# Kernel optimization log

Hardware: AMD Instinct MI355X
Metric: run time of the kernel (lower is better)

## Reference

```python
import jax, jax.numpy as jnp
import numpy as np

B, N, E = 64, 4096, 32768
F_IN, H = 12, 64
K1 = int(np.ceil(0.8 * N))    # TopKPooling ratio=0.8 -> 3277
K2 = int(np.ceil(0.8 * K1))   # -> 2622


def _lin(key, o, i):
    s = 1.0 / np.sqrt(i)
    return jax.random.uniform(key, (o, i), jnp.float32, -s, s)


def setup_inputs() -> dict:
    key = jax.random.key(0)
    ks = jax.random.split(key, 16)
    return {
        "x": jax.random.normal(ks[0], (B, N, F_IN), jnp.float32),
        "edge_index": jax.random.randint(ks[1], (B, 2, E), 0, N),
        # GraphConv 1: lin_rel (with bias) on aggregated msgs, lin_root (no bias)
        "W1_rel": _lin(ks[2], H, F_IN),
        "b1": jnp.zeros((H,), jnp.float32),
        "W1_root": _lin(ks[3], H, F_IN),
        # TopKPooling 1 projection vector
        "p1": jax.random.normal(ks[4], (H,), jnp.float32),
        # GraphConv 2
        "W2_rel": _lin(ks[5], H, H),
        "b2": jnp.zeros((H,), jnp.float32),
        "W2_root": _lin(ks[6], H, H),
        "p2": jax.random.normal(ks[7], (H,), jnp.float32),
        # heads
        "Wa1": _lin(ks[8], 64, 128),
        "ba1": jnp.zeros((64,), jnp.float32),
        "Wa5": _lin(ks[9], 10, 64),
        "ba5": jnp.zeros((10,), jnp.float32),
    }


def _graph_conv(x, src, dst, emask, Wr, br, Wn, n):
    # PyG GraphConv: lin_rel(sum_{j->i} x_j) + lin_root(x_i); masked edges send 0
    msg = x[src] * emask[:, None]                      # [E, d]
    agg = jax.ops.segment_sum(msg, dst, num_segments=n)  # [n, d]
    return agg @ Wr.T + br + x @ Wn.T


def _topk_pool(x, src, dst, emask, p, k):
    # score = x.p/||p||; keep top-k nodes, gate by tanh(score); mask dropped edges
    n = x.shape[0]
    score = (x @ p) / jnp.linalg.norm(p)
    vals, perm = jax.lax.top_k(score, k)
    xk = x[perm] * jnp.tanh(vals)[:, None]
    pos = jnp.full((n,), -1, jnp.int32).at[perm].set(jnp.arange(k, dtype=jnp.int32))
    ns, nd = pos[src], pos[dst]
    valid = (ns >= 0) & (nd >= 0) & (emask > 0)
    return xk, jnp.where(valid, ns, 0), jnp.where(valid, nd, 0), valid.astype(x.dtype)


def reference(x, edge_index, W1_rel, b1, W1_root, p1, W2_rel, b2, W2_root, p2, Wa1, ba1, Wa5, ba5):
    def per_graph(xg, eig):
        src, dst = eig[0], eig[1]
        emask = jnp.ones((src.shape[0],), xg.dtype)
        h = jax.nn.relu(_graph_conv(xg, src, dst, emask, W1_rel, b1, W1_root, N))
        h, src, dst, emask = _topk_pool(h, src, dst, emask, p1, K1)
        x1 = jnp.concatenate([h.max(axis=0), h.mean(axis=0)])   # gmp || gap -> [128]
        h = jax.nn.relu(_graph_conv(h, src, dst, emask, W2_rel, b2, W2_root, K1))
        h, src, dst, emask = _topk_pool(h, src, dst, emask, p2, K2)
        x2 = jnp.concatenate([h.max(axis=0), h.mean(axis=0)])
        return x1 + x2

    feats = jax.vmap(per_graph)(x, edge_index)                  # [B, 128]
    a1 = jax.nn.relu(feats @ Wa1.T + ba1)
    a5 = a1 @ Wa5.T + ba5                                       # [B, 10]
    # F.softmax(dim=0).unsqueeze(0): softmax ACROSS graphs, then add leading dim
    return jax.nn.softmax(a5, axis=0)[None]                     # [1, B, 10]
```

## Files before the change

kernel.cpp:

```cpp
#include <hip/hip_runtime.h>
#include <float.h>
#include <math.h>

#define BB 64
#define NN 4096
#define EE 32768
#define FIN 12
#define HD 64
#define KK1 3277
#define KK2 2622
#define TB1 52
#define RB2 16

__global__ __launch_bounds__(1024) void k_csr(const int* __restrict__ ei,
    int* __restrict__ row_ofs, int* __restrict__ esrc, int g0) {
  __shared__ int cnt[NN];
  __shared__ int part[1024];
  int s = blockIdx.x, g = g0 + s, t = threadIdx.x;
  const int* src = ei + (size_t)g * 2 * EE;
  const int* dst = src + EE;
  for (int i = t; i < NN; i += 1024) cnt[i] = 0;
  __syncthreads();
  for (int e = t; e < EE; e += 1024) atomicAdd(&cnt[dst[e]], 1);
  __syncthreads();
  int c0 = cnt[t * 4], c1 = cnt[t * 4 + 1], c2 = cnt[t * 4 + 2], c3 = cnt[t * 4 + 3];
  int tot = c0 + c1 + c2 + c3;
  part[t] = tot;
  __syncthreads();
  for (int off = 1; off < 1024; off <<= 1) {
    int v = part[t];
    int add = (t >= off) ? part[t - off] : 0;
    __syncthreads();
    part[t] = v + add;
    __syncthreads();
  }
  int base = part[t] - tot;
  int b0 = base, b1 = base + c0, b2 = b1 + c1, b3 = b2 + c2;
  cnt[t * 4] = b0; cnt[t * 4 + 1] = b1; cnt[t * 4 + 2] = b2; cnt[t * 4 + 3] = b3;
  int* RO = row_ofs + (size_t)s * (NN + 1);
  RO[t * 4] = b0; RO[t * 4 + 1] = b1; RO[t * 4 + 2] = b2; RO[t * 4 + 3] = b3;
  if (t == 0) RO[NN] = EE;
  __syncthreads();
  int* ES = esrc + (size_t)s * EE;
  for (int e = t; e < EE; e += 1024) {
    int p = atomicAdd(&cnt[dst[e]], 1);
    ES[p] = src[e];
  }
}

__global__ __launch_bounds__(256, 4) void k_h1f(const float* __restrict__ x,
    const int* __restrict__ row_ofs, const int* __restrict__ esrc,
    const float* __restrict__ W1r, const float* __restrict__ b1,
    const float* __restrict__ W1n, const float* __restrict__ p1,
    float* __restrict__ h1, float* __restrict__ score1, int g0, int G8) {
  __shared__ float sCol[32][257];
  int tid = threadIdx.x;
  int b = blockIdx.x, s, nb;
  if (G8 > 0) { int hi = b >> 3; s = (b & 7) * G8 + hi / 16; nb = hi % 16; }
  else { s = b >> 4; nb = b & 15; }
  int node = nb * 256 + tid;
  int g = g0 + s;
  float nq = 0.f;
#pragma unroll 8
  for (int k = 0; k < 64; k++) nq += p1[k] * p1[k];
  float inv_norm = 1.0f / sqrtf(nq);
  const int* RO = row_ofs + (size_t)s * (NN + 1);
  const int* ES = esrc + (size_t)s * EE;
  const float4* X4 = (const float4*)(x + (size_t)g * NN * FIN);
  int r0 = RO[node], r1 = RO[node + 1];
  float a[FIN];
#pragma unroll
  for (int f = 0; f < FIN; f++) a[f] = 0.f;
  for (int i = r0; i < r1; i++) {
    int so = ES[i];
    float4 v0 = X4[(size_t)so * 3];
    float4 v1 = X4[(size_t)so * 3 + 1];
    float4 v2 = X4[(size_t)so * 3 + 2];
    a[0] += v0.x; a[1] += v0.y; a[2]  += v0.z; a[3]  += v0.w;
    a[4] += v1.x; a[5] += v1.y; a[6]  += v1.z; a[7]  += v1.w;
    a[8] += v2.x; a[9] += v2.y; a[10] += v2.z; a[11] += v2.w;
  }
  float xr[FIN];
  {
    float4 u0 = X4[(size_t)node * 3];
    float4 u1 = X4[(size_t)node * 3 + 1];
    float4 u2 = X4[(size_t)node * 3 + 2];
    xr[0] = u0.x; xr[1] = u0.y; xr[2]  = u0.z; xr[3]  = u0.w;
    xr[4] = u1.x; xr[5] = u1.y; xr[6]  = u1.z; xr[7]  = u1.w;
    xr[8] = u2.x; xr[9] = u2.y; xr[10] = u2.z; xr[11] = u2.w;
  }
  float* hbase = h1 + ((size_t)s * NN + (size_t)nb * 256) * HD;
  float v = 0.f;
  for (int half = 0; half < 2; half++) {
#pragma unroll 4
    for (int k0 = 0; k0 < 32; k0++) {
      int k = half * 32 + k0;
      const float* wr = &W1r[k * FIN];
      const float* wn = &W1n[k * FIN];
      float acc = b1[k];
#pragma unroll
      for (int f = 0; f < FIN; f++) acc += a[f] * wr[f] + xr[f] * wn[f];
      acc = fmaxf(acc, 0.f);
      v += acc * p1[k];
      sCol[k0][tid] = acc;
    }
    __syncthreads();
    float* hb = hbase + half * 32;
    for (int i = tid; i < 256 * 32; i += 256) {
      int nd = i >> 5, c = i & 31;
      hb[(size_t)nd * HD + c] = sCol[c][nd];
    }
    __syncthreads();
  }
  score1[(size_t)s * NN + node] = v * inv_norm;
}

__global__ __launch_bounds__(1024) void k_select(const float* __restrict__ score,
    int scStride, int nvalid, int K, int* __restrict__ sel, int selStride,
    int* __restrict__ pos, int posStride, float* __restrict__ tgo) {
  __shared__ unsigned int keys[4096];
  __shared__ int hist[257];
  __shared__ int part[1024];
  __shared__ unsigned int sh_pref;
  __shared__ int sh_rem;
  int s = blockIdx.x, t = threadIdx.x;
  const float* sc = score + (size_t)s * scStride;
  for (int i = t; i < 4096; i += 1024) {
    unsigned int key = 0u;
    if (i < nvalid) {
      unsigned int bb = __float_as_uint(sc[i]);
      key = (bb & 0x80000000u) ? ~bb : (bb | 0x80000000u);
    }
    keys[i] = key;
  }
  if (t == 0) { sh_pref = 0u; sh_rem = K; }
  __syncthreads();
  for (int sh = 24; sh >= 0; sh -= 8) {
    unsigned int pref = sh_pref;
    int rem = sh_rem;
    if (t < 256) hist[t] = 0;
    __syncthreads();
    for (int i = t; i < 4096; i += 1024) {
      unsigned int u = keys[i];
      bool in = (sh == 24) || ((u >> (sh + 8)) == pref);
      if (in) atomicAdd(&hist[(u >> sh) & 255], 1);
    }
    __syncthreads();
    for (int off = 1; off < 256; off <<= 1) {
      int v = 0;
      if (t < 256) { v = hist[t]; if (t + off < 256) v += hist[t + off]; }
      __syncthreads();
      if (t < 256) hist[t] = v;
      __syncthreads();
    }
    if (t < 256) {
      int ge = hist[t];
      int gt_ = (t == 255) ? 0 : hist[t + 1];
      if (ge >= rem && gt_ < rem) {
        sh_pref = (pref << 8) | (unsigned int)t;
        sh_rem = rem - gt_;
      }
    }
    __syncthreads();
  }
  unsigned int thr = sh_pref;
  int remEq = sh_rem;
  uint4 kk = *(const uint4*)&keys[4 * t];
  int eq0 = (kk.x == thr), eq1 = (kk.y == thr), eq2 = (kk.z == thr), eq3 = (kk.w == thr);
  int eqc = eq0 + eq1 + eq2 + eq3;
  part[t] = eqc;
  __syncthreads();
  for (int off = 1; off < 1024; off <<= 1) {
    int v = part[t];
    int add = (t >= off) ? part[t - off] : 0;
    __syncthreads();
    part[t] = v + add;
    __syncthreads();
  }
  int e_run = part[t] - eqc;
  int kp0 = (kk.x > thr) || (eq0 && (e_run < remEq)); e_run += eq0;
  int kp1 = (kk.y > thr) || (eq1 && (e_run < remEq)); e_run += eq1;
  int kp2 = (kk.z > thr) || (eq2 && (e_run < remEq)); e_run += eq2;
  int kp3 = (kk.w > thr) || (eq3 && (e_run < remEq));
  int kc = kp0 + kp1 + kp2 + kp3;
  __syncthreads();
  part[t] = kc;
  __syncthreads();
  for (int off = 1; off < 1024; off <<= 1) {
    int v = part[t];
    int add = (t >= off) ? part[t - off] : 0;
    __syncthreads();
    part[t] = v + add;
    __syncthreads();
  }
  int r = part[t] - kc;
  int kp[4] = {kp0, kp1, kp2, kp3};
#pragma unroll
  for (int q = 0; q < 4; q++) {
    int i = 4 * t + q;
    if (i < nvalid) {
      if (kp[q]) {
        if (sel) sel[(size_t)s * selStride + r] = i;
        if (pos) pos[(size_t)s * posStride + i] = r;
        if (tgo) tgo[(size_t)s * NN + i] = tanhf(sc[i]);
      } else {
        if (pos) pos[(size_t)s * posStride + i] = -1;
        if (tgo) tgo[(size_t)s * NN + i] = 0.f;
      }
    }
    r += kp[q];
  }
}

__global__ __launch_bounds__(256, 4) void k_fuse(const float* __restrict__ h1,
    const int* __restrict__ row_ofs, const int* __restrict__ esrc,
    const int* __restrict__ sel1, const float* __restrict__ tgo,
    const float* __restrict__ W2r, const float* __restrict__ W2n,
    const float* __restrict__ b2, const float* __restrict__ p2,
    float* __restrict__ h2, float* __restrict__ score2,
    float* __restrict__ pmax, float* __restrict__ psum, int G8) {
  __shared__ float sW[64 * 64];
  __shared__ float sG[64 * 68];
  __shared__ float redm[4][64], reds[4][64];
  int b = blockIdx.x, s, tb;
  if (G8 > 0) { int hi = b >> 3; s = (b & 7) * G8 + hi / TB1; tb = hi % TB1; }
  else { s = b / TB1; tb = b % TB1; }
  int tid = threadIdx.x;
  int j0 = tb * 64;
  int nv = KK1 - j0; if (nv > 64) nv = 64;
  int r = tid >> 2, q = tid & 3;
  bool rv = r < nv;
  int d = 0;
  const float* H = h1 + (size_t)s * NN * HD;
  const float* TG = tgo + (size_t)s * NN;
  float td = 0.f;
  if (rv) {
    d = sel1[(size_t)s * KK1 + j0 + r];
    td = TG[d];
  }
  int rb = (tid >> 4) * 4;
  int c0 = (tid & 15) * 4;
  float acc[4][4];
#pragma unroll
  for (int i = 0; i < 4; i++)
#pragma unroll
    for (int cc = 0; cc < 4; cc++) acc[i][cc] = 0.f;

#pragma unroll 4
  for (int i = tid; i < 64 * 64; i += 256) {
    int k = i >> 6, c = i & 63;
    sW[i] = W2r[c * 64 + k];
  }
  {
    float4 a0 = {0.f,0.f,0.f,0.f}, a1 = a0, a2 = a0, a3 = a0;
    float4 b0 = a0, b1 = a0, b2v_ = a0, b3 = a0;
    if (rv) {
      const int* RO = row_ofs + (size_t)s * (NN + 1);
      const int* ES = esrc + (size_t)s * EE;
      int e0 = RO[d], e1 = RO[d + 1];
      int e = e0;
      for (; e + 2 <= e1; e += 2) {
        int oA = ES[e], oB = ES[e + 1];
        float wA = TG[oA], wB = TG[oB];
        const float4* hA = (const float4*)(H + (size_t)oA * HD + q * 16);
        const float4* hB = (const float4*)(H + (size_t)oB * HD + q * 16);
        float4 vA0 = hA[0], vA1 = hA[1], vA2 = hA[2], vA3 = hA[3];
        float4 vB0 = hB[0], vB1 = hB[1], vB2 = hB[2], vB3 = hB[3];
        a0.x += wA * vA0.x; a0.y += wA * vA0.y; a0.z += wA * vA0.z; a0.w += wA * vA0.w;
        a1.x += wA * vA1.x; a1.y += wA * vA1.y; a1.z += wA * vA1.z; a1.w += wA * vA1.w;
        a2.x += wA * vA2.x; a2.y += wA * vA2.y; a2.z += wA * vA2.z; a2.w += wA * vA2.w;
        a3.x += wA * vA3.x; a3.y += wA * vA3.y; a3.z += wA * vA3.z; a3.w += wA * vA3.w;
        b0.x += wB * vB0.x; b0.y += wB * vB0.y; b0.z += wB * vB0.z; b0.w += wB * vB0.w;
        b1.x += wB * vB1.x; b1.y += wB * vB1.y; b1.z += wB * vB1.z; b1.w += wB * vB1.w;
        b2v_.x += wB * vB2.x; b2v_.y += wB * vB2.y; b2v_.z += wB * vB2.z; b2v_.w += wB * vB2.w;
        b3.x += wB * vB3.x; b3.y += wB * vB3.y; b3.z += wB * vB3.z; b3.w += wB * vB3.w;
      }
      if (e < e1) {
        int o = ES[e];
        float w = TG[o];
        const float4* ho = (const float4*)(H + (size_t)o * HD + q * 16);
        float4 v0 = ho[0], v1 = ho[1], v2 = ho[2], v3 = ho[3];
        a0.x += w * v0.x; a0.y += w * v0.y; a0.z += w * v0.z; a0.w += w * v0.w;
        a1.x += w * v1.x; a1.y += w * v1.y; a1.z += w * v1.z; a1.w += w * v1.w;
        a2.x += w * v2.x; a2.y += w * v2.y; a2.z += w * v2.z; a2.w += w * v2.w;
        a3.x += w * v3.x; a3.y += w * v3.y; a3.z += w * v3.z; a3.w += w * v3.w;
      }
      a0.x += b0.x; a0.y += b0.y; a0.z += b0.z; a0.w += b0.w;
      a1.x += b1.x; a1.y += b1.y; a1.z += b1.z; a1.w += b1.w;
      a2.x += b2v_.x; a2.y += b2v_.y; a2.z += b2v_.z; a2.w += b2v_.w;
      a3.x += b3.x; a3.y += b3.y; a3.z += b3.z; a3.w += b3.w;
    }
    float* gw = &sG[r * 68 + q * 16];
    ((float4*)gw)[0] = a0; ((float4*)gw)[1] = a1;
    ((float4*)gw)[2] = a2; ((float4*)gw)[3] = a3;
  }
  __syncthreads();
#pragma unroll 4
  for (int k = 0; k < 64; k += 4) {
    float4 w0 = *(const float4*)&sW[(k + 0) * 64 + c0];
    float4 w1 = *(const float4*)&sW[(k + 1) * 64 + c0];
    float4 w2 = *(const float4*)&sW[(k + 2) * 64 + c0];
    float4 w3 = *(const float4*)&sW[(k + 3) * 64 + c0];
#pragma unroll
    for (int i = 0; i < 4; i++) {
      float4 g = *(const float4*)&sG[(rb + i) * 68 + k];
      acc[i][0] += g.x * w0.x + g.y * w1.x + g.z * w2.x + g.w * w3.x;
      acc[i][1] += g.x * w0.y + g.y * w1.y + g.z * w2.y + g.w * w3.y;
      acc[i][2] += g.x * w0.z + g.y * w1.z + g.z * w2.z + g.w * w3.z;
      acc[i][3] += g.x * w0.w + g.y * w1.w + g.z * w2.w + g.w * w3.w;
    }
  }
  __syncthreads();
#pragma unroll 4
  for (int i = tid; i < 64 * 64; i += 256) {
    int k = i >> 6, c = i & 63;
    sW[i] = W2n[c * 64 + k];
  }
  {
    float4 s0 = {0.f,0.f,0.f,0.f}, s1 = s0, s2 = s0, s3 = s0;
    if (rv) {
      const float4* hd = (const float4*)(H + (size_t)d * HD + q * 16);
      s0 = hd[0]; s1 = hd[1]; s2 = hd[2]; s3 = hd[3];
      s0.x *= td; s0.y *= td; s0.z *= td; s0.w *= td;
      s1.x *= td; s1.y *= td; s1.z *= td; s1.w *= td;
      s2.x *= td; s2.y *= td; s2.z *= td; s2.w *= td;
      s3.x *= td; s3.y *= td; s3.z *= td; s3.w *= td;
    }
    float* gs = &sG[r * 68 + q * 16];
    ((float4*)gs)[0] = s0; ((float4*)gs)[1] = s1;
    ((float4*)gs)[2] = s2; ((float4*)gs)[3] = s3;
  }
  __syncthreads();
  {
    int c = tid & 63, qq = tid >> 6;
    float mx = -FLT_MAX, sm = 0.f;
    int rend = qq * 16 + 16; if (rend > nv) rend = nv;
    for (int rr = qq * 16; rr < rend; rr++) {
      float v = sG[rr * 68 + c];
      mx = fmaxf(mx, v); sm += v;
    }
    redm[qq][c] = mx; reds[qq][c] = sm;
  }
#pragma unroll 4
  for (int k = 0; k < 64; k += 4) {
    float4 w0 = *(const float4*)&sW[(k + 0) * 64 + c0];
    float4 w1 = *(const float4*)&sW[(k + 1) * 64 + c0];
    float4 w2 = *(const float4*)&sW[(k + 2) * 64 + c0];
    float4 w3 = *(const float4*)&sW[(k + 3) * 64 + c0];
#pragma unroll
    for (int i = 0; i < 4; i++) {
      float4 g = *(const float4*)&sG[(rb + i) * 68 + k];
      acc[i][0] += g.x * w0.x + g.y * w1.x + g.z * w2.x + g.w * w3.x;
      acc[i][1] += g.x * w0.y + g.y * w1.y + g.z * w2.y + g.w * w3.y;
      acc[i][2] += g.x * w0.z + g.y * w1.z + g.z * w2.z + g.w * w3.z;
      acc[i][3] += g.x * w0.w + g.y * w1.w + g.z * w2.w + g.w * w3.w;
    }
  }
  __syncthreads();
  if (tid < 64) {
    float mx = redm[0][tid], sm = reds[0][tid];
    for (int qq = 1; qq < 4; qq++) { mx = fmaxf(mx, redm[qq][tid]); sm += reds[qq][tid]; }
    pmax[((size_t)s * TB1 + tb) * 64 + tid] = mx;
    psum[((size_t)s * TB1 + tb) * 64 + tid] = sm;
  }
  float4 b2v = *(const float4*)&b2[c0];
  float4 p2v = *(const float4*)&p2[c0];
  float nq = p2v.x * p2v.x + p2v.y * p2v.y + p2v.z * p2v.z + p2v.w * p2v.w;
  nq += __shfl_xor(nq, 1, 64);
  nq += __shfl_xor(nq, 2, 64);
  nq += __shfl_xor(nq, 4, 64);
  nq += __shfl_xor(nq, 8, 64);
  float inv_norm = 1.0f / sqrtf(nq);
  float vs[4];
#pragma unroll
  for (int i = 0; i < 4; i++) {
    int j = j0 + rb + i;
    float4 h;
    h.x = fmaxf(acc[i][0] + b2v.x, 0.f);
    h.y = fmaxf(acc[i][1] + b2v.y, 0.f);
    h.z = fmaxf(acc[i][2] + b2v.z, 0.f);
    h.w = fmaxf(acc[i][3] + b2v.w, 0.f);
    if (j < KK1) *(float4*)&h2[((size_t)s * KK1 + j) * 64 + c0] = h;
    vs[i] = h.x * p2v.x + h.y * p2v.y + h.z * p2v.z + h.w * p2v.w;
  }
#pragma unroll
  for (int i = 0; i < 4; i++) {
    vs[i] += __shfl_xor(vs[i], 1, 64);
    vs[i] += __shfl_xor(vs[i], 2, 64);
    vs[i] += __shfl_xor(vs[i], 4, 64);
    vs[i] += __shfl_xor(vs[i], 8, 64);
  }
  if ((tid & 15) == 0) {
#pragma unroll
    for (int i = 0; i < 4; i++) {
      int j = j0 + rb + i;
      if (j < KK1) score2[(size_t)s * KK1 + j] = vs[i] * inv_norm;
    }
  }
}

__global__ __launch_bounds__(64) void k_read1r(const float* __restrict__ pmax,
    const float* __restrict__ psum, float* __restrict__ x1) {
  int s = blockIdx.x, k = threadIdx.x;
  float mx = -FLT_MAX, sm = 0.f;
  for (int t = 0; t < TB1; t++) {
    mx = fmaxf(mx, pmax[((size_t)s * TB1 + t) * 64 + k]);
    sm += psum[((size_t)s * TB1 + t) * 64 + k];
  }
  x1[(size_t)s * 128 + k] = mx;
  x1[(size_t)s * 128 + 64 + k] = sm / (float)KK1;
}

__global__ __launch_bounds__(256) void k_read2p(const float* __restrict__ h2,
    const int* __restrict__ pos2, const float* __restrict__ score2,
    float* __restrict__ p2max, float* __restrict__ p2sum) {
  int s = blockIdx.x / RB2, pb = blockIdx.x % RB2;
  int lane = threadIdx.x & 63, wave = threadIdx.x >> 6;
  const int ROWS = (KK1 + RB2 - 1) / RB2;
  int j0 = pb * ROWS;
  int j1 = j0 + ROWS; if (j1 > KK1) j1 = KK1;
  float mx = -FLT_MAX, sm = 0.f;
  for (int j = j0 + wave; j < j1; j += 4) {
    if (pos2[(size_t)s * KK1 + j] >= 0) {
      float t = tanhf(score2[(size_t)s * KK1 + j]);
      float v = h2[((size_t)s * KK1 + j) * HD + lane] * t;
      mx = fmaxf(mx, v); sm += v;
    }
  }
  __shared__ float smx[4][64], ssm[4][64];
  smx[wave][lane] = mx; ssm[wave][lane] = sm;
  __syncthreads();
  if (wave == 0) {
    for (int q = 1; q < 4; q++) { mx = fmaxf(mx, smx[q][lane]); sm += ssm[q][lane]; }
    p2max[((size_t)s * RB2 + pb) * 64 + lane] = mx;
    p2sum[((size_t)s * RB2 + pb) * 64 + lane] = sm;
  }
}

__global__ __launch_bounds__(64) void k_read2r(const float* __restrict__ p2max,
    const float* __restrict__ p2sum, const float* __restrict__ x1,
    float* __restrict__ feats, int g0) {
  int s = blockIdx.x, k = threadIdx.x;
  float mx = -FLT_MAX, sm = 0.f;
  for (int t = 0; t < RB2; t++) {
    mx = fmaxf(mx, p2max[((size_t)s * RB2 + t) * 64 + k]);
    sm += p2sum[((size_t)s * RB2 + t) * 64 + k];
  }
  feats[(size_t)(g0 + s) * 128 + k] = x1[(size_t)s * 128 + k] + mx;
  feats[(size_t)(g0 + s) * 128 + 64 + k] = x1[(size_t)s * 128 + 64 + k] + sm / (float)KK2;
}

__global__ __launch_bounds__(256) void k_heada(const float* __restrict__ feats,
    const float* __restrict__ Wa1, const float* __restrict__ ba1,
    const float* __restrict__ Wa5, const float* __restrict__ ba5,
    float* __restrict__ a5) {
  __shared__ float sF[128];
  __shared__ float sA1[64];
  int b = blockIdx.x, t = threadIdx.x;
  if (t < 32) ((float4*)sF)[t] = ((const float4*)(feats + (size_t)b * 128))[t];
  __syncthreads();
  {
    int j = t >> 2, q = t & 3;
    const float4* w = (const float4*)(Wa1 + (size_t)j * 128 + q * 32);
    const float4* f4 = (const float4*)(sF + q * 32);
    float acc = 0.f;
#pragma unroll
    for (int i = 0; i < 8; i++) {
      float4 wv = w[i], fv = f4[i];
      acc += wv.x * fv.x + wv.y * fv.y + wv.z * fv.z + wv.w * fv.w;
    }
    acc += __shfl_xor(acc, 1, 64);
    acc += __shfl_xor(acc, 2, 64);
    if (q == 0) sA1[j] = fmaxf(acc + ba1[j], 0.f);
  }
  __syncthreads();
  if (t < 160) {
    int c = t >> 4, l = t & 15;
    float acc = 0.f;
#pragma unroll
    for (int i = 0; i < 4; i++) {
      int jj = l * 4 + i;
      acc += sA1[jj] * Wa5[c * 64 + jj];
    }
    acc += __shfl_xor(acc, 1, 64);
    acc += __shfl_xor(acc, 2, 64);
    acc += __shfl_xor(acc, 4, 64);
    acc += __shfl_xor(acc, 8, 64);
    if (l == 0) a5[b * 10 + c] = acc + ba5[c];
  }
}

__global__ __launch_bounds__(64) void k_headb(const float* __restrict__ a5,
    float* __restrict__ out) {
  int c = threadIdx.x;
  if (c < 10) {
    float m = -FLT_MAX;
    for (int b = 0; b < BB; b++) m = fmaxf(m, a5[b * 10 + c]);
    float sum = 0.f;
    for (int b = 0; b < BB; b++) sum += expf(a5[b * 10 + c] - m);
    float inv = 1.0f / sum;
    for (int b = 0; b < BB; b++) out[b * 10 + c] = expf(a5[b * 10 + c] - m) * inv;
  }
}

extern "C" void kernel_launch(void* const* d_in, const int* in_sizes, int n_in,
                              void* d_out, int out_size, void* d_ws, size_t ws_size,
                              hipStream_t stream) {
  const float* x   = (const float*)d_in[0];
  const int*   ei  = (const int*)d_in[1];
  const float* W1r = (const float*)d_in[2];
  const float* b1  = (const float*)d_in[3];
  const float* W1n = (const float*)d_in[4];
  const float* p1  = (const float*)d_in[5];
  const float* W2r = (const float*)d_in[6];
  const float* b2  = (const float*)d_in[7];
  const float* W2n = (const float*)d_in[8];
  const float* p2  = (const float*)d_in[9];
  const float* Wa1 = (const float*)d_in[10];
  const float* ba1 = (const float*)d_in[11];
  const float* Wa5 = (const float*)d_in[12];
  const float* ba5 = (const float*)d_in[13];
  float* out = (float*)d_out;

  char* base = (char*)d_ws;
  size_t off = 0;
  auto alloc = [&](size_t bytes) -> void* {
    void* p = base + off;
    off = (off + bytes + 255) & ~(size_t)255;
    return p;
  };
  float* feats = (float*)alloc((size_t)BB * 128 * 4);
  float* a5buf = (float*)alloc((size_t)BB * 10 * 4);

  const size_t perSlot =
      ((size_t)(NN + 1) + EE + (size_t)NN * HD + NN + KK1 + NN +
       (size_t)KK1 * HD + 2 * (size_t)KK1 +
       2 * (size_t)TB1 * 64 + 2 * (size_t)RB2 * 64 + 128) * 4
      + 24 * 256;
  size_t avail = ws_size > off ? ws_size - off : 0;
  int CH = (int)(avail / perSlot);
  if (CH > BB) CH = BB;
  if (CH < 1) CH = 1;

  int*   row_ofs = (int*)alloc((size_t)CH * (NN + 1) * 4);
  int*   esrc    = (int*)alloc((size_t)CH * EE * 4);
  float* h1      = (float*)alloc((size_t)CH * NN * HD * 4);
  float* score1  = (float*)alloc((size_t)CH * NN * 4);
  int*   sel1    = (int*)alloc((size_t)CH * KK1 * 4);
  float* tgo     = (float*)alloc((size_t)CH * NN * 4);
  float* h2      = (float*)alloc((size_t)CH * KK1 * HD * 4);
  float* score2  = (float*)alloc((size_t)CH * KK1 * 4);
  int*   pos2    = (int*)alloc((size_t)CH * KK1 * 4);
  float* pmax    = (float*)alloc((size_t)CH * TB1 * 64 * 4);
  float* psum    = (float*)alloc((size_t)CH * TB1 * 64 * 4);
  float* p2max   = (float*)alloc((size_t)CH * RB2 * 64 * 4);
  float* p2sum   = (float*)alloc((size_t)CH * RB2 * 64 * 4);
  float* x1      = (float*)alloc((size_t)CH * 128 * 4);

  for (int g0 = 0; g0 < BB; g0 += CH) {
    int G = (BB - g0) < CH ? (BB - g0) : CH;
    int G8 = (G % 8 == 0) ? G / 8 : 0;
    k_csr<<<G, 1024, 0, stream>>>(ei, row_ofs, esrc, g0);
    k_h1f<<<G * 16, 256, 0, stream>>>(x, row_ofs, esrc, W1r, b1, W1n, p1, h1, score1, g0, G8);
    k_select<<<G, 1024, 0, stream>>>(score1, NN, NN, KK1, sel1, KK1, nullptr, 0, tgo);
    k_fuse<<<G * TB1, 256, 0, stream>>>(h1, row_ofs, esrc, sel1, tgo, W2r, W2n, b2, p2,
                                        h2, score2, pmax, psum, G8);
    k_select<<<G, 1024, 0, stream>>>(score2, KK1, KK1, KK2, nullptr, 0, pos2, KK1, nullptr);
    k_read1r<<<G, 64, 0, stream>>>(pmax, psum, x1);
    k_read2p<<<G * RB2, 256, 0, stream>>>(h2, pos2, score2, p2max, p2sum);
    k_read2r<<<G, 64, 0, stream>>>(p2max, p2sum, x1, feats, g0);
  }
  k_heada<<<BB, 256, 0, stream>>>(feats, Wa1, ba1, Wa5, ba5, a5buf);
  k_headb<<<1, 64, 0, stream>>>(a5buf, out);
}
```

Baseline: 296.3 us.

## Halve k_fuse weight LDS, skip second prefix scan, merge readout kernels

k_fuse now stages the 64x64 weight matrices into shared memory in two 32-row halves, with extra barriers between them. This shrinks LDS per block so the launch bound can rise to five blocks per CU. k_select skips its second prefix scan when no sel output is requested and writes pos as 0 or -1, which works only if the consumer treats pos as a keep flag. The two readout reduction kernels are merged into one, removing a launch and the x1 buffer, at the cost of more synchronization in k_fuse.

```diff
diff --git a/kernel.cpp b/kernel.cpp
--- a/kernel.cpp
+++ b/kernel.cpp
@@ -182,44 +182,55 @@
   int kp1 = (kk.y > thr) || (eq1 && (e_run < remEq)); e_run += eq1;
   int kp2 = (kk.z > thr) || (eq2 && (e_run < remEq)); e_run += eq2;
   int kp3 = (kk.w > thr) || (eq3 && (e_run < remEq));
-  int kc = kp0 + kp1 + kp2 + kp3;
-  __syncthreads();
-  part[t] = kc;
-  __syncthreads();
-  for (int off = 1; off < 1024; off <<= 1) {
-    int v = part[t];
-    int add = (t >= off) ? part[t - off] : 0;
-    __syncthreads();
-    part[t] = v + add;
-    __syncthreads();
-  }
-  int r = part[t] - kc;
   int kp[4] = {kp0, kp1, kp2, kp3};
-#pragma unroll
-  for (int q = 0; q < 4; q++) {
-    int i = 4 * t + q;
-    if (i < nvalid) {
-      if (kp[q]) {
-        if (sel) sel[(size_t)s * selStride + r] = i;
-        if (pos) pos[(size_t)s * posStride + i] = r;
-        if (tgo) tgo[(size_t)s * NN + i] = tanhf(sc[i]);
-      } else {
-        if (pos) pos[(size_t)s * posStride + i] = -1;
-        if (tgo) tgo[(size_t)s * NN + i] = 0.f;
+  if (sel) {
+    int kc = kp0 + kp1 + kp2 + kp3;
+    __syncthreads();
+    part[t] = kc;
+    __syncthreads();
+    for (int off = 1; off < 1024; off <<= 1) {
+      int v = part[t];
+      int add = (t >= off) ? part[t - off] : 0;
+      __syncthreads();
+      part[t] = v + add;
+      __syncthreads();
+    }
+    int r = part[t] - kc;
+#pragma unroll
+    for (int q = 0; q < 4; q++) {
+      int i = 4 * t + q;
+      if (i < nvalid) {
+        if (kp[q]) {
+          sel[(size_t)s * selStride + r] = i;
+          if (pos) pos[(size_t)s * posStride + i] = r;
+          if (tgo) tgo[(size_t)s * NN + i] = tanhf(sc[i]);
+        } else {
+          if (pos) pos[(size_t)s * posStride + i] = -1;
+          if (tgo) tgo[(size_t)s * NN + i] = 0.f;
+        }
       }
-    }
-    r += kp[q];
-  }
-}
-
-__global__ __launch_bounds__(256, 4) void k_fuse(const float* __restrict__ h1,
+      r += kp[q];
+    }
+  } else {
+#pragma unroll
+    for (int q = 0; q < 4; q++) {
+      int i = 4 * t + q;
+      if (i < nvalid) {
+        if (pos) pos[(size_t)s * posStride + i] = kp[q] ? 0 : -1;
+        if (tgo) tgo[(size_t)s * NN + i] = kp[q] ? tanhf(sc[i]) : 0.f;
+      }
+    }
+  }
+}
+
+__global__ __launch_bounds__(256, 5) void k_fuse(const float* __restrict__ h1,
     const int* __restrict__ row_ofs, const int* __restrict__ esrc,
     const int* __restrict__ sel1, const float* __restrict__ tgo,
     const float* __restrict__ W2r, const float* __restrict__ W2n,
     const float* __restrict__ b2, const float* __restrict__ p2,
     float* __restrict__ h2, float* __restrict__ score2,
     float* __restrict__ pmax, float* __restrict__ psum, int G8) {
-  __shared__ float sW[64 * 64];
+  __shared__ float sW[32 * 64];
   __shared__ float sG[64 * 68];
   __shared__ float redm[4][64], reds[4][64];
   int b = blockIdx.x, s, tb;
@@ -246,11 +257,30 @@
 #pragma unroll
     for (int cc = 0; cc < 4; cc++) acc[i][cc] = 0.f;
 
-#pragma unroll 4
-  for (int i = tid; i < 64 * 64; i += 256) {
-    int k = i >> 6, c = i & 63;
-    sW[i] = W2r[c * 64 + k];
-  }
+#define STAGE_W(Wsrc, kbase)                                   \
+  _Pragma("unroll 4")                                          \
+  for (int i = tid; i < 32 * 64; i += 256) {                   \
+    int k = i >> 6, c = i & 63;                                \
+    sW[i] = (Wsrc)[c * 64 + (kbase) + k];                      \
+  }
+#define GEMM_SEG(gofs)                                         \
+  _Pragma("unroll 4")                                          \
+  for (int k = 0; k < 32; k += 4) {                            \
+    float4 w0 = *(const float4*)&sW[(k + 0) * 64 + c0];        \
+    float4 w1 = *(const float4*)&sW[(k + 1) * 64 + c0];        \
+    float4 w2 = *(const float4*)&sW[(k + 2) * 64 + c0];        \
+    float4 w3 = *(const float4*)&sW[(k + 3) * 64 + c0];        \
+    _Pragma("unroll")                                          \
+    for (int i = 0; i < 4; i++) {                              \
+      float4 g = *(const float4*)&sG[(rb + i) * 68 + (gofs) + k]; \
+      acc[i][0] += g.x * w0.x + g.y * w1.x + g.z * w2.x + g.w * w3.x; \
+      acc[i][1] += g.x * w0.y + g.y * w1.y + g.z * w2.y + g.w * w3.y; \
+      acc[i][2] += g.x * w0.z + g.y * w1.z + g.z * w2.z + g.w * w3.z; \
+      acc[i][3] += g.x * w0.w + g.y * w1.w + g.z * w2.w + g.w * w3.w; \
+    }                                                          \
+  }
+
+  STAGE_W(W2r, 0)
   {
     float4 a0 = {0.f,0.f,0.f,0.f}, a1 = a0, a2 = a0, a3 = a0;
     float4 b0 = a0, b1 = a0, b2v_ = a0, b3 = a0;
@@ -295,27 +325,13 @@
     ((float4*)gw)[2] = a2; ((float4*)gw)[3] = a3;
   }
   __syncthreads();
-#pragma unroll 4
-  for (int k = 0; k < 64; k += 4) {
-    float4 w0 = *(const float4*)&sW[(k + 0) * 64 + c0];
-    float4 w1 = *(const float4*)&sW[(k + 1) * 64 + c0];
-    float4 w2 = *(const float4*)&sW[(k + 2) * 64 + c0];
-    float4 w3 = *(const float4*)&sW[(k + 3) * 64 + c0];
-#pragma unroll
-    for (int i = 0; i < 4; i++) {
-      float4 g = *(const float4*)&sG[(rb + i) * 68 + k];
-      acc[i][0] += g.x * w0.x + g.y * w1.x + g.z * w2.x + g.w * w3.x;
-      acc[i][1] += g.x * w0.y + g.y * w1.y + g.z * w2.y + g.w * w3.y;
-      acc[i][2] += g.x * w0.z + g.y * w1.z + g.z * w2.z + g.w * w3.z;
-      acc[i][3] += g.x * w0.w + g.y * w1.w + g.z * w2.w + g.w * w3.w;
-    }
-  }
-  __syncthreads();
-#pragma unroll 4
-  for (int i = tid; i < 64 * 64; i += 256) {
-    int k = i >> 6, c = i & 63;
-    sW[i] = W2n[c * 64 + k];
-  }
+  GEMM_SEG(0)
+  __syncthreads();
+  STAGE_W(W2r, 32)
+  __syncthreads();
+  GEMM_SEG(32)
+  __syncthreads();
+  STAGE_W(W2n, 0)
   {
     float4 s0 = {0.f,0.f,0.f,0.f}, s1 = s0, s2 = s0, s3 = s0;
     if (rv) {
@@ -341,28 +357,19 @@
     }
     redm[qq][c] = mx; reds[qq][c] = sm;
   }
-#pragma unroll 4
-  for (int k = 0; k < 64; k += 4) {
-    float4 w0 = *(const float4*)&sW[(k + 0) * 64 + c0];
-    float4 w1 = *(const float4*)&sW[(k + 1) * 64 + c0];
-    float4 w2 = *(const float4*)&sW[(k + 2) * 64 + c0];
-    float4 w3 = *(const float4*)&sW[(k + 3) * 64 + c0];
-#pragma unroll
-    for (int i = 0; i < 4; i++) {
-      float4 g = *(const float4*)&sG[(rb + i) * 68 + k];
-      acc[i][0] += g.x * w0.x + g.y * w1.x + g.z * w2.x + g.w * w3.x;
-      acc[i][1] += g.x * w0.y + g.y * w1.y + g.z * w2.y + g.w * w3.y;
-      acc[i][2] += g.x * w0.z + g.y * w1.z + g.z * w2.z + g.w * w3.z;
-      acc[i][3] += g.x * w0.w + g.y * w1.w + g.z * w2.w + g.w * w3.w;
-    }
-  }
-  __syncthreads();
+  GEMM_SEG(0)
+  __syncthreads();
+  STAGE_W(W2n, 32)
   if (tid < 64) {
     float mx = redm[0][tid], sm = reds[0][tid];
     for (int qq = 1; qq < 4; qq++) { mx = fmaxf(mx, redm[qq][tid]); sm += reds[qq][tid]; }
     pmax[((size_t)s * TB1 + tb) * 64 + tid] = mx;
     psum[((size_t)s * TB1 + tb) * 64 + tid] = sm;
   }
+  __syncthreads();
+  GEMM_SEG(32)
+#undef STAGE_W
+#undef GEMM_SEG
   float4 b2v = *(const float4*)&b2[c0];
   float4 p2v = *(const float4*)&p2[c0];
   float nq = p2v.x * p2v.x + p2v.y * p2v.y + p2v.z * p2v.z + p2v.w * p2v.w;
@@ -397,18 +404,6 @@
       if (j < KK1) score2[(size_t)s * KK1 + j] = vs[i] * inv_norm;
     }
   }
-}
-
-__global__ __launch_bounds__(64) void k_read1r(const float* __restrict__ pmax,
-    const float* __restrict__ psum, float* __restrict__ x1) {
-  int s = blockIdx.x, k = threadIdx.x;
-  float mx = -FLT_MAX, sm = 0.f;
-  for (int t = 0; t < TB1; t++) {
-    mx = fmaxf(mx, pmax[((size_t)s * TB1 + t) * 64 + k]);
-    sm += psum[((size_t)s * TB1 + t) * 64 + k];
-  }
-  x1[(size_t)s * 128 + k] = mx;
-  x1[(size_t)s * 128 + 64 + k] = sm / (float)KK1;
 }
 
 __global__ __launch_bounds__(256) void k_read2p(const float* __restrict__ h2,
@@ -437,17 +432,22 @@
   }
 }
 
-__global__ __launch_bounds__(64) void k_read2r(const float* __restrict__ p2max,
-    const float* __restrict__ p2sum, const float* __restrict__ x1,
-    float* __restrict__ feats, int g0) {
+__global__ __launch_bounds__(64) void k_readf(const float* __restrict__ pmax,
+    const float* __restrict__ psum, const float* __restrict__ p2max,
+    const float* __restrict__ p2sum, float* __restrict__ feats, int g0) {
   int s = blockIdx.x, k = threadIdx.x;
-  float mx = -FLT_MAX, sm = 0.f;
+  float mx1 = -FLT_MAX, sm1 = 0.f;
+  for (int t = 0; t < TB1; t++) {
+    mx1 = fmaxf(mx1, pmax[((size_t)s * TB1 + t) * 64 + k]);
+    sm1 += psum[((size_t)s * TB1 + t) * 64 + k];
+  }
+  float mx2 = -FLT_MAX, sm2 = 0.f;
   for (int t = 0; t < RB2; t++) {
-    mx = fmaxf(mx, p2max[((size_t)s * RB2 + t) * 64 + k]);
-    sm += p2sum[((size_t)s * RB2 + t) * 64 + k];
-  }
-  feats[(size_t)(g0 + s) * 128 + k] = x1[(size_t)s * 128 + k] + mx;
-  feats[(size_t)(g0 + s) * 128 + 64 + k] = x1[(size_t)s * 128 + 64 + k] + sm / (float)KK2;
+    mx2 = fmaxf(mx2, p2max[((size_t)s * RB2 + t) * 64 + k]);
+    sm2 += p2sum[((size_t)s * RB2 + t) * 64 + k];
+  }
+  feats[(size_t)(g0 + s) * 128 + k] = mx1 + mx2;
+  feats[(size_t)(g0 + s) * 128 + 64 + k] = sm1 / (float)KK1 + sm2 / (float)KK2;
 }
 
 __global__ __launch_bounds__(256) void k_heada(const float* __restrict__ feats,
@@ -535,7 +535,7 @@
   const size_t perSlot =
       ((size_t)(NN + 1) + EE + (size_t)NN * HD + NN + KK1 + NN +
        (size_t)KK1 * HD + 2 * (size_t)KK1 +
-       2 * (size_t)TB1 * 64 + 2 * (size_t)RB2 * 64 + 128) * 4
+       2 * (size_t)TB1 * 64 + 2 * (size_t)RB2 * 64) * 4
       + 24 * 256;
   size_t avail = ws_size > off ? ws_size - off : 0;
   int CH = (int)(avail / perSlot);
@@ -555,7 +555,6 @@
   float* psum    = (float*)alloc((size_t)CH * TB1 * 64 * 4);
   float* p2max   = (float*)alloc((size_t)CH * RB2 * 64 * 4);
   float* p2sum   = (float*)alloc((size_t)CH * RB2 * 64 * 4);
-  float* x1      = (float*)alloc((size_t)CH * 128 * 4);
 
   for (int g0 = 0; g0 < BB; g0 += CH) {
     int G = (BB - g0) < CH ? (BB - g0) : CH;
@@ -566,9 +565,8 @@
     k_fuse<<<G * TB1, 256, 0, stream>>>(h1, row_ofs, esrc, sel1, tgo, W2r, W2n, b2, p2,
                                         h2, score2, pmax, psum, G8);
     k_select<<<G, 1024, 0, stream>>>(score2, KK1, KK1, KK2, nullptr, 0, pos2, KK1, nullptr);
-    k_read1r<<<G, 64, 0, stream>>>(pmax, psum, x1);
     k_read2p<<<G * RB2, 256, 0, stream>>>(h2, pos2, score2, p2max, p2sum);
-    k_read2r<<<G, 64, 0, stream>>>(p2max, p2sum, x1, feats, g0);
+    k_readf<<<G, 64, 0, stream>>>(pmax, psum, p2max, p2sum, feats, g0);
   }
   k_heada<<<BB, 256, 0, stream>>>(feats, Wa1, ba1, Wa5, ba5, a5buf);
   k_headb<<<1, 64, 0, stream>>>(a5buf, out);
```

New measurement: 293.9 us, median of 2. Within noise of the previous version (-0.8%).
